# Kernel optimization log

Measured on AMD Instinct MI355X. Metric: run time of the kernel, lower is better.

## Reference

```python
import jax, jax.numpy as jnp
import numpy as np

TIME_STEPS = 50
LEFT_PAD = 250 // TIME_STEPS            # 5
MAX_DELAY = LEFT_PAD if LEFT_PAD % 2 == 1 else LEFT_PAD + 1  # 5 (odd)
SIG = float(MAX_DELAY // 2)             # 2.0, frozen
CIN = 34 * 34 * 2                       # 2312
HID = 300
NOUT = 10
BETA = 0.9
THRESH = 1.0
BATCH = 128


def setup_inputs() -> dict:
    key = jax.random.key(0)
    k = jax.random.split(key, 6)
    data = jax.random.normal(k[0], (BATCH, TIME_STEPS, CIN), jnp.float32)
    W1 = jax.random.normal(k[1], (HID, CIN), jnp.float32) / np.sqrt(CIN * MAX_DELAY).astype(np.float32)
    P1 = jax.random.uniform(k[2], (HID, CIN), jnp.float32, -SIG, SIG)
    b1 = jnp.zeros((HID,), jnp.float32)
    W2 = jax.random.normal(k[3], (NOUT, HID), jnp.float32) / np.sqrt(HID * MAX_DELAY).astype(np.float32)
    P2 = jax.random.uniform(k[4], (NOUT, HID), jnp.float32, -SIG, SIG)
    b2 = jnp.zeros((NOUT,), jnp.float32)
    return {"data": data, "W1": W1, "P1": P1, "b1": b1, "W2": W2, "P2": P2, "b2": b2}


def make_gauss_kernel(W, P):
    # DCLS 'gauss': weight W placed at learnable position P (centered at KS//2)
    # with Gaussian of width SIG, normalized over the KS taps. kernel_count=1.
    idx = jnp.arange(MAX_DELAY, dtype=W.dtype)              # [KS]
    c = P[..., None] + (MAX_DELAY // 2)                     # [O, I, 1]
    g = jnp.exp(-0.5 * ((idx - c) / SIG) ** 2)              # [O, I, KS]
    g = g / (g.sum(-1, keepdims=True) + 1e-7)
    return W[..., None] * g                                 # [O, I, KS]


def delay_conv(x, W, P, b):
    # x: [B, Cin, L], valid conv with synthesized kernel -> [B, Cout, L-KS+1]
    K = make_gauss_kernel(W, P)
    y = jax.lax.conv_general_dilated(x, K, window_strides=(1,), padding='VALID',
                                     dimension_numbers=('NCH', 'OIH', 'NCH'))
    return y + b[None, :, None]


def lif_scan(x):
    # snntorch Leaky (reset-by-subtraction, reset detached):
    #   mem_t = beta*mem_{t-1} + x_t - H(mem_{t-1}-thr)*thr ;  spk_t = H(mem_t-thr)
    # x: [B, C, T] -> (spk [T,B,C], mem [T,B,C])
    def step(mem, xt):
        reset = (mem > THRESH).astype(xt.dtype)
        mem_new = BETA * mem + xt - reset * THRESH
        spk = (mem_new > THRESH).astype(xt.dtype)
        return mem_new, (spk, mem_new)

    xs = jnp.moveaxis(x, 2, 0)                              # [T, B, C]
    mem0 = jnp.zeros(x.shape[:2], x.dtype)
    _, (spks, mems) = jax.lax.scan(step, mem0, xs)
    return spks, mems


def reference(data, W1, P1, b1, W2, P2, b2):
    # pad time (dim -2) on the left, permute to [B, Cin, T+pad]
    x = jnp.pad(data, ((0, 0), (LEFT_PAD, 0), (0, 0)))
    x = jnp.transpose(x, (0, 2, 1))                         # [B, CIN, T+pad]
    x = delay_conv(x, W1, P1, b1)                           # [B, HID, T1]
    spk1, _ = lif_scan(x)                                   # [T1, B, HID]
    h = jnp.moveaxis(spk1, 0, 2)                            # [B, HID, T1]
    h = jnp.pad(h, ((0, 0), (0, 0), (LEFT_PAD, 0)))
    y = delay_conv(h, W2, P2, b2)                           # [B, NOUT, T2]
    spk2, mem2 = lif_scan(y)                                # [T2, B, NOUT] each
    return spk2, mem2
```

## Files before the change

kernel.cpp:

```cpp
#include <hip/hip_runtime.h>

#define BSZ  128
#define TT   50
#define CIN  2312
#define HID  300
#define NOUT 10
#define KS   5
#define T1   51
#define T2   52

#define NC32 73
#define KFRAG_U 20480

typedef unsigned int u32;
typedef unsigned short u16;
typedef __attribute__((ext_vector_type(8))) short s16x8;
typedef __attribute__((ext_vector_type(4))) float f32x4;

#define EK1f 0.88249690258459546f
#define EK2f 0.60653065971263342f
#define EK3f 0.32465246735834974f
#define EK4f 0.13533528323661270f

static __device__ __forceinline__ u16 bfhi(float x) {
  u32 u = __float_as_uint(x);
  return (u16)((u + 0x7fffu + ((u >> 16) & 1u)) >> 16);
}
static __device__ __forceinline__ float bf2f(u16 h) {
  return __uint_as_float(((u32)h) << 16);
}

__global__ __launch_bounds__(256) void snn_prepm(
    const float* __restrict__ W1, const float* __restrict__ P1,
    u16* __restrict__ K1bf)
{
  const int c  = blockIdx.x;
  const int ow = blockIdx.y;
  const int tid = threadIdx.x;
  const int nt = tid >> 6, ll = tid & 63;
  const int g = ll >> 4, lr = ll & 15;
  const int o  = ow * 64 + nt * 16 + lr;
  const int ib = c * 32 + g * 8;

  s16x8 hv[5], lv[5];
#pragma unroll
  for (int k = 0; k < 5; ++k)
#pragma unroll
    for (int j = 0; j < 8; ++j) { hv[k][j] = 0; lv[k][j] = 0; }

  if (o < HID) {
    const float* wrow = W1 + (size_t)o * CIN;
    const float* prow = P1 + (size_t)o * CIN;
#pragma unroll
    for (int j = 0; j < 8; ++j) {
      const int i = ib + j;
      if (i < CIN) {
        const float w1 = wrow[i], p1 = prow[i];
        const float cc = p1 + 2.0f;
        const float E0 = __expf(-0.125f * cc * cc);
        const float U  = __expf(0.25f * cc);
        const float u2 = U * U;
        const float e0 = E0;
        const float e1 = E0 * U * EK1f;
        const float e2 = E0 * u2 * EK2f;
        const float e3 = E0 * (u2 * U) * EK3f;
        const float e4 = E0 * (u2 * u2) * EK4f;
        const float inv = 1.0f / (((((e0 + e1) + e2) + e3) + e4) + 1e-7f);
        const float vk[5] = { w1 * (e0 * inv), w1 * (e1 * inv),
                              w1 * (e2 * inv), w1 * (e3 * inv),
                              w1 * (e4 * inv) };
#pragma unroll
        for (int k = 0; k < 5; ++k) {
          const u16 h = bfhi(vk[k]);
          const u16 lo = bfhi(vk[k] - bf2f(h));
          hv[k][j] = (short)h; lv[k][j] = (short)lo;
        }
      }
    }
  }
  u16* base = K1bf + ((size_t)ow * NC32 + c) * KFRAG_U + nt * 1024 + ll * 8;
#pragma unroll
  for (int k = 0; k < 5; ++k) {
    *(s16x8*)(base + k * 4096)       = hv[k];
    *(s16x8*)(base + k * 4096 + 512) = lv[k];
  }
}

__global__ __launch_bounds__(256, 2) void snn_l1m(
    const float* __restrict__ data, const u16* __restrict__ K1bf,
    const float* __restrict__ b1v, u32* __restrict__ gbits)
{
  __shared__ double dsm[3264];
  u16* A16 = (u16*)dsm;

  const int tid = threadIdx.x;
  const int bid = blockIdx.x;
  const int rnk = (bid & 7) * 80 + (bid >> 3);
  const int ow = rnk >> 7;
  const int b  = rnk & 127;

  const int w  = tid >> 6, l = tid & 63;
  const int lr = l & 15, lg = l >> 4;
  const int wr = w >> 1, wc = w & 1;
  const int abase_u = (32 * wr + lr) * 40 + lg * 8;

  const float* dbase = data + (size_t)b * (TT * CIN);
  const u16* kb = K1bf + (size_t)ow * NC32 * KFRAG_U + l * 8;
  const int ntg0 = wc * 2, ntg1 = wc * 2 + 1;

  const int s1 = tid >> 2;
  const int j4 = tid & 3;
  const int tp = s1 - 5;
  const bool avld = (tp >= 0) && (tp < TT);
  const float* aptr = dbase + (size_t)(avld ? tp : 0) * CIN + j4 * 8;

#define LDB(c_, k_, ntg_, h_) \
  (*(const s16x8*)(kb + (size_t)(c_) * KFRAG_U + (k_) * 4096 + (ntg_) * 1024 + (h_) * 512))

  s16x8 bh[5][2], bl[5][2];
#pragma unroll
  for (int k = 0; k < 5; ++k) {
    bh[k][0] = LDB(0, k, ntg0, 0); bh[k][1] = LDB(0, k, ntg1, 0);
    bl[k][0] = LDB(0, k, ntg0, 1); bl[k][1] = LDB(0, k, ntg1, 1);
  }

  float4 ra0, ra1;
  {
    ra0 = avld ? *(const float4*)(aptr)     : make_float4(0.f, 0.f, 0.f, 0.f);
    ra1 = avld ? *(const float4*)(aptr + 4) : make_float4(0.f, 0.f, 0.f, 0.f);
  }

  if (tid < 80) {
    s16x8 z;
#pragma unroll
    for (int j = 0; j < 8; ++j) z[j] = 0;
    const int r = tid / 20, off = (tid % 20) * 8;
    *(s16x8*)(A16 + r * 2720 + 2560 + off) = z;
  }

  {
    const float f[8] = { ra0.x, ra0.y, ra0.z, ra0.w,
                         ra1.x, ra1.y, ra1.z, ra1.w };
    s16x8 hv, lv;
#pragma unroll
    for (int j = 0; j < 8; ++j) {
      const u16 h = bfhi(f[j]);
      hv[j] = (short)h;
      lv[j] = (short)bfhi(f[j] - bf2f(h));
    }
    *(s16x8*)(A16 + s1 * 40 + j4 * 8) = hv;
    *(s16x8*)(A16 + 2720 + s1 * 40 + j4 * 8) = lv;
  }
  {
    const bool iv = avld;
    const float* p = aptr + 32;
    ra0 = iv ? *(const float4*)(p)     : make_float4(0.f, 0.f, 0.f, 0.f);
    ra1 = iv ? *(const float4*)(p + 4) : make_float4(0.f, 0.f, 0.f, 0.f);
  }
  __syncthreads();

  f32x4 accf[2][2];
  double accd[2][2][4];
#pragma unroll
  for (int m = 0; m < 2; ++m)
#pragma unroll
    for (int n = 0; n < 2; ++n)
#pragma unroll
      for (int q = 0; q < 4; ++q) { accf[m][n][q] = 0.f; accd[m][n][q] = 0.0; }

  int p = 0;
  for (int c = 0; c < NC32; ++c) {
    u16* bufC = A16 + p * 2720 * 2;
    u16* bufN = A16 + (p ^ 1) * 2720 * 2;

    if (c + 1 < NC32) {
      const float f[8] = { ra0.x, ra0.y, ra0.z, ra0.w,
                           ra1.x, ra1.y, ra1.z, ra1.w };
      s16x8 hv, lv;
#pragma unroll
      for (int j = 0; j < 8; ++j) {
        const u16 h = bfhi(f[j]);
        hv[j] = (short)h;
        lv[j] = (short)bfhi(f[j] - bf2f(h));
      }
      *(s16x8*)(bufN + s1 * 40 + j4 * 8) = hv;
      *(s16x8*)(bufN + 2720 + s1 * 40 + j4 * 8) = lv;

      const int cn = (c + 2 < NC32) ? c + 2 : NC32 - 1;
      const bool iv = avld && ((cn < 72) || (j4 == 0));
      const float* pp = aptr + cn * 32;
      ra0 = iv ? *(const float4*)(pp)     : make_float4(0.f, 0.f, 0.f, 0.f);
      ra1 = iv ? *(const float4*)(pp + 4) : make_float4(0.f, 0.f, 0.f, 0.f);
    }

    const int cb = (c + 1 < NC32) ? c + 1 : c;
#pragma unroll
    for (int k = 0; k < 5; ++k) {
      const s16x8 ah0 = *(const s16x8*)(bufC + abase_u + k * 40);
      const s16x8 al0 = *(const s16x8*)(bufC + 2720 + abase_u + k * 40);
      const s16x8 ah1 = *(const s16x8*)(bufC + abase_u + (16 + k) * 40);
      const s16x8 al1 = *(const s16x8*)(bufC + 2720 + abase_u + (16 + k) * 40);

      accf[0][0] = __builtin_amdgcn_mfma_f32_16x16x32_bf16(ah0, bh[k][0], accf[0][0], 0, 0, 0);
      accf[0][0] = __builtin_amdgcn_mfma_f32_16x16x32_bf16(al0, bh[k][0], accf[0][0], 0, 0, 0);
      accf[0][0] = __builtin_amdgcn_mfma_f32_16x16x32_bf16(ah0, bl[k][0], accf[0][0], 0, 0, 0);

      accf[0][1] = __builtin_amdgcn_mfma_f32_16x16x32_bf16(ah0, bh[k][1], accf[0][1], 0, 0, 0);
      accf[0][1] = __builtin_amdgcn_mfma_f32_16x16x32_bf16(al0, bh[k][1], accf[0][1], 0, 0, 0);
      accf[0][1] = __builtin_amdgcn_mfma_f32_16x16x32_bf16(ah0, bl[k][1], accf[0][1], 0, 0, 0);

      accf[1][0] = __builtin_amdgcn_mfma_f32_16x16x32_bf16(ah1, bh[k][0], accf[1][0], 0, 0, 0);
      accf[1][0] = __builtin_amdgcn_mfma_f32_16x16x32_bf16(al1, bh[k][0], accf[1][0], 0, 0, 0);
      accf[1][0] = __builtin_amdgcn_mfma_f32_16x16x32_bf16(ah1, bl[k][0], accf[1][0], 0, 0, 0);

      accf[1][1] = __builtin_amdgcn_mfma_f32_16x16x32_bf16(ah1, bh[k][1], accf[1][1], 0, 0, 0);
      accf[1][1] = __builtin_amdgcn_mfma_f32_16x16x32_bf16(al1, bh[k][1], accf[1][1], 0, 0, 0);
      accf[1][1] = __builtin_amdgcn_mfma_f32_16x16x32_bf16(ah1, bl[k][1], accf[1][1], 0, 0, 0);

      bh[k][0] = LDB(cb, k, ntg0, 0); bh[k][1] = LDB(cb, k, ntg1, 0);
      bl[k][0] = LDB(cb, k, ntg0, 1); bl[k][1] = LDB(cb, k, ntg1, 1);
    }

#pragma unroll
    for (int m = 0; m < 2; ++m)
#pragma unroll
      for (int n = 0; n < 2; ++n)
#pragma unroll
        for (int q = 0; q < 4; ++q) {
          accd[m][n][q] += (double)accf[m][n][q];
          accf[m][n][q] = 0.f;
        }
    __syncthreads();
    p ^= 1;
  }
#undef LDB

  double* y1s = dsm;
#pragma unroll
  for (int m = 0; m < 2; ++m)
#pragma unroll
    for (int n = 0; n < 2; ++n)
#pragma unroll
      for (int q = 0; q < 4; ++q) {
        const int t = 32 * wr + 16 * m + lg * 4 + q;
        if (t < T1) y1s[t * 64 + 32 * wc + 16 * n + lr] = accd[m][n][q];
      }
  __syncthreads();

  if (tid < 64) {
    const int o = ow * 64 + tid;
    const bool valid = o < HID;
    const double bias = valid ? (double)b1v[o] : 0.0;
    u32* bits = gbits + (size_t)b * 510;
    double mem = 0.0;
    for (int t = 0; t < T1; ++t) {
      const double x = y1s[t * 64 + tid] + bias;
      const double reset = (mem > 1.0) ? 1.0 : 0.0;
      mem = __dsub_rn(__dadd_rn(__dmul_rn(0.9, mem), x), reset);
      const unsigned long long mk = __ballot(valid && (mem > 1.0));
      if (tid == 0)  bits[t * 10 + 2 * ow]     = (u32)mk;
      if (tid == 32) bits[t * 10 + 2 * ow + 1] = (u32)(mk >> 32);
    }
  }
}

__device__ __forceinline__ void layer1_tile_g(
    int b, int ow, int tid,
    const float* __restrict__ data, const float* __restrict__ W1,
    const float* __restrict__ P1, const float* __restrict__ b1v,
    double* __restrict__ dsm, u32* __restrict__ bits)
{
  float* Bsf = (float*)dsm;
  float* As  = (float*)dsm + 2880;

  const int ty = tid >> 5;
  const int tx = tid & 31;
  const int r0 = ty << 3;
  const int c0 = tx << 1;

  const float* abase = data + (size_t)b * (TT * CIN);

  const int slot = tid >> 2;
  const int pair = tid & 3;
  const int tp   = slot - 5;

  const int isub = tid & 7;
  const int oA = tid >> 3;
  const int oB = oA + 32;
  const int boA = ow * 64 + oA;
  const int boB = ow * 64 + oB;
  const bool vB = boB < HID;

  double acc[8][2];
#pragma unroll
  for (int r = 0; r < 8; ++r) { acc[r][0] = 0.0; acc[r][1] = 0.0; }

  float2 aA = make_float2(0.f, 0.f);
  float wA = 0.f, pA = 0.f, wB = 0.f, pB = 0.f;
  if (tid < 220 && tp >= 0)
    aA = *(const float2*)(abase + (size_t)tp * CIN + 2 * pair);
  wA = W1[(size_t)boA * CIN + isub];
  pA = P1[(size_t)boA * CIN + isub];
  if (vB) {
    wB = W1[(size_t)boB * CIN + isub];
    pB = P1[(size_t)boB * CIN + isub];
  }

  for (int i0 = 0; i0 < CIN; i0 += 8) {
    if (tid < 220) {
      As[(2 * pair) * 80 + slot]     = aA.x;
      As[(2 * pair + 1) * 80 + slot] = aA.y;
    }
    {
      const float c  = pA + 2.0f;
      const float E0 = __expf(-0.125f * c * c);
      const float U  = __expf(0.25f * c);
      const float u2 = U * U;
      const float e0 = E0;
      const float e1 = E0 * U * EK1f;
      const float e2 = E0 * u2 * EK2f;
      const float e3 = E0 * (u2 * U) * EK3f;
      const float e4 = E0 * (u2 * u2) * EK4f;
      const float inv = 1.0f / (((((e0 + e1) + e2) + e3) + e4) + 1e-7f);
      float* bp = Bsf + isub * 72 + oA;
      bp[0]    = wA * (e0 * inv);
      bp[576]  = wA * (e1 * inv);
      bp[1152] = wA * (e2 * inv);
      bp[1728] = wA * (e3 * inv);
      bp[2304] = wA * (e4 * inv);
    }
    {
      const float c  = pB + 2.0f;
      const float E0 = __expf(-0.125f * c * c);
      const float U  = __expf(0.25f * c);
      const float u2 = U * U;
      const float e0 = E0;
      const float e1 = E0 * U * EK1f;
      const float e2 = E0 * u2 * EK2f;
      const float e3 = E0 * (u2 * U) * EK3f;
      const float e4 = E0 * (u2 * u2) * EK4f;
      const float inv = 1.0f / (((((e0 + e1) + e2) + e3) + e4) + 1e-7f);
      float* bp = Bsf + isub * 72 + oB;
      bp[0]    = wB * (e0 * inv);
      bp[576]  = wB * (e1 * inv);
      bp[1152] = wB * (e2 * inv);
      bp[1728] = wB * (e3 * inv);
      bp[2304] = wB * (e4 * inv);
    }
    __syncthreads();

    const int i0n = i0 + 8;
    if (i0n < CIN) {
      if (tid < 220 && tp >= 0)
        aA = *(const float2*)(abase + (size_t)tp * CIN + i0n + 2 * pair);
      wA = W1[(size_t)boA * CIN + i0n + isub];
      pA = P1[(size_t)boA * CIN + i0n + isub];
      if (vB) {
        wB = W1[(size_t)boB * CIN + i0n + isub];
        pB = P1[(size_t)boB * CIN + i0n + isub];
      }
    }

    float accf[8][2];
#pragma unroll
    for (int r = 0; r < 8; ++r) { accf[r][0] = 0.f; accf[r][1] = 0.f; }
#pragma unroll
    for (int kk = 0; kk < 8; ++kk) {
      const float* ap = &As[kk * 80 + r0];
      const float4 a0 = *(const float4*)(ap);
      const float4 a1 = *(const float4*)(ap + 4);
      const float4 a2 = *(const float4*)(ap + 8);
      float av[12];
      av[0] = a0.x; av[1] = a0.y; av[2]  = a0.z; av[3]  = a0.w;
      av[4] = a1.x; av[5] = a1.y; av[6]  = a1.z; av[7]  = a1.w;
      av[8] = a2.x; av[9] = a2.y; av[10] = a2.z; av[11] = a2.w;
      float bv[KS][2];
#pragma unroll
      for (int k = 0; k < KS; ++k) {
        const float2 bb = *(const float2*)&Bsf[(k * 8 + kk) * 72 + c0];
        bv[k][0] = bb.x; bv[k][1] = bb.y;
      }
#pragma unroll
      for (int k = 0; k < KS; ++k)
#pragma unroll
        for (int r = 0; r < 8; ++r) {
          accf[r][0] = fmaf(av[r + k], bv[k][0], accf[r][0]);
          accf[r][1] = fmaf(av[r + k], bv[k][1], accf[r][1]);
        }
    }
#pragma unroll
    for (int r = 0; r < 8; ++r) {
      acc[r][0] += (double)accf[r][0];
      acc[r][1] += (double)accf[r][1];
    }
    __syncthreads();
  }

  double* y1s = dsm;
#pragma unroll
  for (int r = 0; r < 8; ++r) {
    const int t = r0 + r;
    if (t < T1) {
      y1s[t * 64 + c0]     = acc[r][0];
      y1s[t * 64 + c0 + 1] = acc[r][1];
    }
  }
  __syncthreads();

  if (tid < 64) {
    const int o = ow * 64 + tid;
    const bool valid = o < HID;
    const double bias = valid ? (double)b1v[o] : 0.0;
    double mem = 0.0;
    for (int t = 0; t < T1; ++t) {
      const double x = y1s[t * 64 + tid] + bias;
      const double reset = (mem > 1.0) ? 1.0 : 0.0;
      mem = __dsub_rn(__dadd_rn(__dmul_rn(0.9, mem), x), reset);
      const unsigned long long mk = __ballot(valid && (mem > 1.0));
      if (tid == 0)  bits[t * 10 + 2 * ow]     = (u32)mk;
      if (tid == 32) bits[t * 10 + 2 * ow + 1] = (u32)(mk >> 32);
    }
  }
  __syncthreads();
}

__device__ __forceinline__ void layer2_lif2(
    int b, int tid, float* smem,
    const float* __restrict__ W2, const float* __restrict__ P2,
    const float* __restrict__ b2, float* __restrict__ out)
{
  float* K2s = smem;
  const u32* lbits = (const u32*)(smem + 15000);
  float* y2s = smem + 15510;

  for (int idx = tid; idx < NOUT * HID; idx += 256) {
    const int o = idx / HID, i = idx % HID;
    const float w = W2[idx], p = P2[idx];
    const float c = p + 2.0f;
    float e[KS], s = 0.f;
#pragma unroll
    for (int k = 0; k < KS; ++k) {
      const float d = ((float)k - c) * 0.5f;
      e[k] = __expf(-0.5f * d * d);
      s += e[k];
    }
    const float denom = s + 1e-7f;
#pragma unroll
    for (int k = 0; k < KS; ++k)
      K2s[(o * KS + k) * HID + i] = w * (e[k] / denom);
  }
  __syncthreads();

  for (int task = tid; task < T2 * NOUT; task += 256) {
    const int t2 = task / NOUT, o = task % NOUT;
    float acc = b2[o];
#pragma unroll
    for (int k = 0; k < KS; ++k) {
      const int tp = t2 + k - KS;
      if (tp < 0 || tp >= T1) continue;
      const float* kr = K2s + (o * KS + k) * HID;
      const u32* br = lbits + tp * 10;
      for (int i = 0; i < HID; ++i)
        acc = fmaf((float)((br[i >> 5] >> (i & 31)) & 1u), kr[i], acc);
    }
    y2s[task] = acc;
  }
  __syncthreads();

  if (tid < NOUT) {
    float mem = 0.f;
    for (int t = 0; t < T2; ++t) {
      const float x = y2s[t * NOUT + tid];
      const float reset = (mem > 1.0f) ? 1.0f : 0.0f;
      mem = __fsub_rn(__fadd_rn(__fmul_rn(0.9f, mem), x), reset);
      out[(size_t)t * (BSZ * NOUT) + b * NOUT + tid] = (mem > 1.0f) ? 1.0f : 0.0f;
      out[(size_t)T2 * BSZ * NOUT + (size_t)t * (BSZ * NOUT) + b * NOUT + tid] = mem;
    }
  }
}

__global__ __launch_bounds__(256) void snn_l1(
    const float* __restrict__ data, const float* __restrict__ W1,
    const float* __restrict__ P1, const float* __restrict__ b1v,
    u32* __restrict__ gbits)
{
  __shared__ double dsm[3264];
  const int ow = blockIdx.x, b = blockIdx.y;
  layer1_tile_g(b, ow, threadIdx.x, data, W1, P1, b1v, dsm,
                gbits + (size_t)b * 510);
}

__global__ __launch_bounds__(256) void snn_l2k(
    const u32* __restrict__ gbits,
    const float* __restrict__ W2, const float* __restrict__ P2,
    const float* __restrict__ b2, float* __restrict__ out)
{
  __shared__ float smem[16030];
  const int b = blockIdx.x, tid = threadIdx.x;
  u32* lbits = (u32*)(smem + 15000);
  for (int i = tid; i < 510; i += 256) lbits[i] = gbits[(size_t)b * 510 + i];
  layer2_lif2(b, tid, smem, W2, P2, b2, out);
}

__global__ __launch_bounds__(256) void snn_mono(
    const float* __restrict__ data, const float* __restrict__ W1,
    const float* __restrict__ P1, const float* __restrict__ b1v,
    const float* __restrict__ W2, const float* __restrict__ P2,
    const float* __restrict__ b2, float* __restrict__ out)
{
  __shared__ double dsm[8015];
  const int b = blockIdx.x, tid = threadIdx.x;
  u32* lbits = (u32*)((float*)dsm + 15000);
  for (int ow = 0; ow < 5; ++ow)
    layer1_tile_g(b, ow, tid, data, W1, P1, b1v, dsm, lbits);
  layer2_lif2(b, tid, (float*)dsm, W2, P2, b2, out);
}

extern "C" void kernel_launch(void* const* d_in, const int* in_sizes, int n_in,
                              void* d_out, int out_size, void* d_ws, size_t ws_size,
                              hipStream_t stream) {
  const float* data = (const float*)d_in[0];
  const float* W1   = (const float*)d_in[1];
  const float* P1   = (const float*)d_in[2];
  const float* b1v  = (const float*)d_in[3];
  const float* W2   = (const float*)d_in[4];
  const float* P2   = (const float*)d_in[5];
  const float* b2   = (const float*)d_in[6];
  float* out = (float*)d_out;

  const size_t BITS_BYTES = (size_t)BSZ * T1 * 10 * sizeof(u32);
  const size_t K1_OFF = 262144;
  const size_t K1BF_BYTES = (size_t)5 * NC32 * KFRAG_U * 2;
  const size_t NEED_M = K1_OFF + K1BF_BYTES;

  if (ws_size >= NEED_M) {
    u32* gbits = (u32*)d_ws;
    u16* K1bf  = (u16*)((char*)d_ws + K1_OFF);
    snn_prepm<<<dim3(NC32, 5), 256, 0, stream>>>(W1, P1, K1bf);
    snn_l1m<<<640, 256, 0, stream>>>(data, K1bf, b1v, gbits);
    snn_l2k<<<BSZ, 256, 0, stream>>>(gbits, W2, P2, b2, out);
  } else if (ws_size >= BITS_BYTES) {
    u32* gbits = (u32*)d_ws;
    snn_l1<<<dim3(5, BSZ), 256, 0, stream>>>(data, W1, P1, b1v, gbits);
    snn_l2k<<<BSZ, 256, 0, stream>>>(gbits, W2, P2, b2, out);
  } else {
    snn_mono<<<BSZ, 256, 0, stream>>>(data, W1, P1, b1v, W2, P2, b2, out);
  }
}
```

Measured before the change: 401.4 us.

## Split layer-1 channel reduction in two and move LIF1 into layer-2 kernel

Adds a split-K variant of the layer-1 MFMA kernel that divides the 73 channel chunks between two blocks, launching 1280 blocks with a higher occupancy hint. Each block writes float partial sums to a workspace buffer. A new layer-2 kernel adds the two partials plus bias, runs the layer-1 LIF scan in double precision, and then does layer 2. The aim is more parallelism and better CU coverage for the large GEMM. The cost is extra global traffic for the partials, and rounding the per-half double accumulators to float could flip spikes near threshold. The old kernel is also tidied into the same load/stage macro structure.

New measurement: 984.7 us. +145.3%, slower.

```diff
diff --git a/kernel.cpp b/kernel.cpp
--- a/kernel.cpp
+++ b/kernel.cpp
@@ -86,6 +86,244 @@
   }
 }
 
+__global__ __launch_bounds__(256, 4) void snn_l1s(
+    const float* __restrict__ data, const u16* __restrict__ K1bf,
+    float* __restrict__ pbuf)
+{
+  __shared__ __align__(16) double dsm[2720];
+  u16* A16 = (u16*)dsm;
+
+  const int tid = threadIdx.x;
+  const int bid = blockIdx.x;
+  const int g  = bid & 7;
+  const int r  = bid >> 3;
+  const int s  = r & 1;
+  const int u  = r >> 1;
+  const int x  = g * 80 + u;
+  const int ow = x >> 7;
+  const int b  = x & 127;
+
+  const int c_lo = s ? 37 : 0;
+  const int c_hi = s ? 73 : 37;
+
+  const int w  = tid >> 6, l = tid & 63;
+  const int lr = l & 15, lg = l >> 4;
+  const int wr = w >> 1, wc = w & 1;
+  const int abase_u = (32 * wr + lr) * 40 + lg * 8;
+
+  const float* dbase = data + (size_t)b * (TT * CIN);
+  const u16* kbn = K1bf + (size_t)ow * NC32 * KFRAG_U + l * 8;
+  const int ntg0 = wc * 2, ntg1 = wc * 2 + 1;
+
+  const int s1 = tid >> 2;
+  const int j4 = tid & 3;
+  const int tp = s1 - 5;
+  const bool avld = (tp >= 0) && (tp < TT);
+  const float* aptr = dbase + (size_t)(avld ? tp : 0) * CIN + j4 * 8;
+
+  if (tid < 80) {
+    s16x8 z;
+#pragma unroll
+    for (int j = 0; j < 8; ++j) z[j] = 0;
+    const int rr = tid / 20, off = (tid % 20) * 8;
+    *(s16x8*)(A16 + rr * 2720 + 2560 + off) = z;
+  }
+
+#define LOADA(CC)                                                             \
+  {                                                                           \
+    const bool iv_ = avld && (((CC) < 72) || (j4 == 0));                      \
+    const float* pp_ = aptr + (size_t)(CC) * 32;                              \
+    ra0 = iv_ ? *(const float4*)(pp_)     : make_float4(0.f, 0.f, 0.f, 0.f);  \
+    ra1 = iv_ ? *(const float4*)(pp_ + 4) : make_float4(0.f, 0.f, 0.f, 0.f);  \
+  }
+
+#define STAGE_A(CC)                                                           \
+  {                                                                           \
+    const float f_[8] = { ra0.x, ra0.y, ra0.z, ra0.w,                         \
+                          ra1.x, ra1.y, ra1.z, ra1.w };                       \
+    s16x8 hv_, lv_;                                                           \
+    _Pragma("unroll")                                                         \
+    for (int j = 0; j < 8; ++j) {                                             \
+      const u16 h_ = bfhi(f_[j]);                                             \
+      hv_[j] = (short)h_;                                                     \
+      lv_[j] = (short)bfhi(f_[j] - bf2f(h_));                                 \
+    }                                                                         \
+    u16* bn_ = A16 + ((CC) & 1) * 5440;                                       \
+    const int woff_ = s1 * 40 + j4 * 8;                                       \
+    *(s16x8*)(bn_ + woff_) = hv_;                                             \
+    *(s16x8*)(bn_ + 2720 + woff_) = lv_;                                      \
+  }
+
+  s16x8 bh[5][2], bl[5][2];
+#pragma unroll
+  for (int k = 0; k < 5; ++k) {
+    const u16* cb_ = kbn + (size_t)c_lo * KFRAG_U + k * 4096;
+    bh[k][0] = *(const s16x8*)(cb_ + ntg0 * 1024);
+    bh[k][1] = *(const s16x8*)(cb_ + ntg1 * 1024);
+    bl[k][0] = *(const s16x8*)(cb_ + ntg0 * 1024 + 512);
+    bl[k][1] = *(const s16x8*)(cb_ + ntg1 * 1024 + 512);
+  }
+
+  f32x4 accf[2][2];
+  double accd[2][2][4];
+#pragma unroll
+  for (int m = 0; m < 2; ++m)
+#pragma unroll
+    for (int n = 0; n < 2; ++n)
+#pragma unroll
+      for (int q = 0; q < 4; ++q) { accf[m][n][q] = 0.f; accd[m][n][q] = 0.0; }
+
+  float4 ra0, ra1;
+  LOADA(c_lo);
+  STAGE_A(c_lo);
+  LOADA(c_lo + 1);
+  __syncthreads();
+
+  for (int c = c_lo; c < c_hi; ++c) {
+    if (c + 1 < c_hi) {
+      STAGE_A(c + 1);
+      if (c + 2 < c_hi) LOADA(c + 2);
+    }
+
+    {
+      const u16* bc_ = A16 + (c & 1) * 5440;
+      const int rc = c + 1;
+#pragma unroll
+      for (int k = 0; k < 5; ++k) {
+        const s16x8 ah0 = *(const s16x8*)(bc_ + abase_u + k * 40);
+        const s16x8 al0 = *(const s16x8*)(bc_ + 2720 + abase_u + k * 40);
+        const s16x8 ah1 = *(const s16x8*)(bc_ + abase_u + (16 + k) * 40);
+        const s16x8 al1 = *(const s16x8*)(bc_ + 2720 + abase_u + (16 + k) * 40);
+
+        accf[0][0] = __builtin_amdgcn_mfma_f32_16x16x32_bf16(ah0, bh[k][0], accf[0][0], 0, 0, 0);
+        accf[0][0] = __builtin_amdgcn_mfma_f32_16x16x32_bf16(al0, bh[k][0], accf[0][0], 0, 0, 0);
+        accf[0][0] = __builtin_amdgcn_mfma_f32_16x16x32_bf16(ah0, bl[k][0], accf[0][0], 0, 0, 0);
+
+        accf[0][1] = __builtin_amdgcn_mfma_f32_16x16x32_bf16(ah0, bh[k][1], accf[0][1], 0, 0, 0);
+        accf[0][1] = __builtin_amdgcn_mfma_f32_16x16x32_bf16(al0, bh[k][1], accf[0][1], 0, 0, 0);
+        accf[0][1] = __builtin_amdgcn_mfma_f32_16x16x32_bf16(ah0, bl[k][1], accf[0][1], 0, 0, 0);
+
+        accf[1][0] = __builtin_amdgcn_mfma_f32_16x16x32_bf16(ah1, bh[k][0], accf[1][0], 0, 0, 0);
+        accf[1][0] = __builtin_amdgcn_mfma_f32_16x16x32_bf16(al1, bh[k][0], accf[1][0], 0, 0, 0);
+        accf[1][0] = __builtin_amdgcn_mfma_f32_16x16x32_bf16(ah1, bl[k][0], accf[1][0], 0, 0, 0);
+
+        accf[1][1] = __builtin_amdgcn_mfma_f32_16x16x32_bf16(ah1, bh[k][1], accf[1][1], 0, 0, 0);
+        accf[1][1] = __builtin_amdgcn_mfma_f32_16x16x32_bf16(al1, bh[k][1], accf[1][1], 0, 0, 0);
+        accf[1][1] = __builtin_amdgcn_mfma_f32_16x16x32_bf16(ah1, bl[k][1], accf[1][1], 0, 0, 0);
+
+        if (rc < c_hi) {
+          const u16* cb_ = kbn + (size_t)rc * KFRAG_U + k * 4096;
+          bh[k][0] = *(const s16x8*)(cb_ + ntg0 * 1024);
+          bh[k][1] = *(const s16x8*)(cb_ + ntg1 * 1024);
+          bl[k][0] = *(const s16x8*)(cb_ + ntg0 * 1024 + 512);
+          bl[k][1] = *(const s16x8*)(cb_ + ntg1 * 1024 + 512);
+        }
+      }
+    }
+
+#pragma unroll
+    for (int m = 0; m < 2; ++m)
+#pragma unroll
+      for (int n = 0; n < 2; ++n)
+#pragma unroll
+        for (int q = 0; q < 4; ++q) {
+          accd[m][n][q] += (double)accf[m][n][q];
+          accf[m][n][q] = 0.f;
+        }
+    __syncthreads();
+  }
+#undef LOADA
+#undef STAGE_A
+
+  float* pb = pbuf + (((size_t)s * 5 + ow) * 128 + b) * 3264;
+#pragma unroll
+  for (int m = 0; m < 2; ++m)
+#pragma unroll
+    for (int n = 0; n < 2; ++n)
+#pragma unroll
+      for (int q = 0; q < 4; ++q) {
+        const int t = 32 * wr + 16 * m + lg * 4 + q;
+        if (t < T1) pb[t * 64 + 32 * wc + 16 * n + lr] = (float)accd[m][n][q];
+      }
+}
+
+__global__ __launch_bounds__(256) void snn_l2m(
+    const float* __restrict__ pbuf, const float* __restrict__ b1v,
+    const float* __restrict__ W2, const float* __restrict__ P2,
+    const float* __restrict__ b2, float* __restrict__ out)
+{
+  __shared__ float smem[16030];
+  const int b = blockIdx.x, tid = threadIdx.x;
+  float* K2s = smem;
+  u32* lbits = (u32*)(smem + 15000);
+  float* y2s = smem + 15510;
+
+  for (int idx = tid; idx < NOUT * HID; idx += 256) {
+    const int o = idx / HID, i = idx % HID;
+    const float w = W2[idx], p = P2[idx];
+    const float c = p + 2.0f;
+    float e[KS], ssum = 0.f;
+#pragma unroll
+    for (int k = 0; k < KS; ++k) {
+      const float d = ((float)k - c) * 0.5f;
+      e[k] = __expf(-0.5f * d * d);
+      ssum += e[k];
+    }
+    const float denom = ssum + 1e-7f;
+#pragma unroll
+    for (int k = 0; k < KS; ++k)
+      K2s[(o * KS + k) * HID + i] = w * (e[k] / denom);
+  }
+
+  {
+    const int w = tid >> 6, l = tid & 63;
+    for (int ow = w; ow < 5; ow += 4) {
+      const int o = ow * 64 + l;
+      const bool valid = o < HID;
+      const double bias = valid ? (double)b1v[o] : 0.0;
+      const float* p0 = pbuf + (((size_t)0 * 5 + ow) * 128 + b) * 3264 + l;
+      const float* p1 = pbuf + (((size_t)1 * 5 + ow) * 128 + b) * 3264 + l;
+      double mem = 0.0;
+      for (int t = 0; t < T1; ++t) {
+        const double x = (double)p0[t * 64] + (double)p1[t * 64] + bias;
+        const double reset = (mem > 1.0) ? 1.0 : 0.0;
+        mem = __dsub_rn(__dadd_rn(__dmul_rn(0.9, mem), x), reset);
+        const unsigned long long mk = __ballot(valid && (mem > 1.0));
+        if (l == 0)  lbits[t * 10 + 2 * ow]     = (u32)mk;
+        if (l == 32) lbits[t * 10 + 2 * ow + 1] = (u32)(mk >> 32);
+      }
+    }
+  }
+  __syncthreads();
+
+  for (int task = tid; task < T2 * NOUT; task += 256) {
+    const int t2 = task / NOUT, o = task % NOUT;
+    float acc = b2[o];
+#pragma unroll
+    for (int k = 0; k < KS; ++k) {
+      const int tp = t2 + k - KS;
+      if (tp < 0 || tp >= T1) continue;
+      const float* kr = K2s + (o * KS + k) * HID;
+      const u32* br = lbits + tp * 10;
+      for (int i = 0; i < HID; ++i)
+        acc = fmaf((float)((br[i >> 5] >> (i & 31)) & 1u), kr[i], acc);
+    }
+    y2s[task] = acc;
+  }
+  __syncthreads();
+
+  if (tid < NOUT) {
+    float mem = 0.f;
+    for (int t = 0; t < T2; ++t) {
+      const float x = y2s[t * NOUT + tid];
+      const float reset = (mem > 1.0f) ? 1.0f : 0.0f;
+      mem = __fsub_rn(__fadd_rn(__fmul_rn(0.9f, mem), x), reset);
+      out[(size_t)t * (BSZ * NOUT) + b * NOUT + tid] = (mem > 1.0f) ? 1.0f : 0.0f;
+      out[(size_t)T2 * BSZ * NOUT + (size_t)t * (BSZ * NOUT) + b * NOUT + tid] = mem;
+    }
+  }
+}
+
 __global__ __launch_bounds__(256, 2) void snn_l1m(
     const float* __restrict__ data, const u16* __restrict__ K1bf,
     const float* __restrict__ b1v, u32* __restrict__ gbits)
@@ -105,7 +343,7 @@
   const int abase_u = (32 * wr + lr) * 40 + lg * 8;
 
   const float* dbase = data + (size_t)b * (TT * CIN);
-  const u16* kb = K1bf + (size_t)ow * NC32 * KFRAG_U + l * 8;
+  const u16* kbn = K1bf + (size_t)ow * NC32 * KFRAG_U + l * 8;
   const int ntg0 = wc * 2, ntg1 = wc * 2 + 1;
 
   const int s1 = tid >> 2;
@@ -114,50 +352,48 @@
   const bool avld = (tp >= 0) && (tp < TT);
   const float* aptr = dbase + (size_t)(avld ? tp : 0) * CIN + j4 * 8;
 
-#define LDB(c_, k_, ntg_, h_) \
-  (*(const s16x8*)(kb + (size_t)(c_) * KFRAG_U + (k_) * 4096 + (ntg_) * 1024 + (h_) * 512))
-
-  s16x8 bh[5][2], bl[5][2];
-#pragma unroll
-  for (int k = 0; k < 5; ++k) {
-    bh[k][0] = LDB(0, k, ntg0, 0); bh[k][1] = LDB(0, k, ntg1, 0);
-    bl[k][0] = LDB(0, k, ntg0, 1); bl[k][1] = LDB(0, k, ntg1, 1);
-  }
-
-  float4 ra0, ra1;
-  {
-    ra0 = avld ? *(const float4*)(aptr)     : make_float4(0.f, 0.f, 0.f, 0.f);
-    ra1 = avld ? *(const float4*)(aptr + 4) : make_float4(0.f, 0.f, 0.f, 0.f);
-  }
-
   if (tid < 80) {
     s16x8 z;
 #pragma unroll
     for (int j = 0; j < 8; ++j) z[j] = 0;
-    const int r = tid / 20, off = (tid % 20) * 8;
-    *(s16x8*)(A16 + r * 2720 + 2560 + off) = z;
-  }
-
-  {
-    const float f[8] = { ra0.x, ra0.y, ra0.z, ra0.w,
-                         ra1.x, ra1.y, ra1.z, ra1.w };
-    s16x8 hv, lv;
-#pragma unroll
-    for (int j = 0; j < 8; ++j) {
-      const u16 h = bfhi(f[j]);
-      hv[j] = (short)h;
-      lv[j] = (short)bfhi(f[j] - bf2f(h));
-    }
-    *(s16x8*)(A16 + s1 * 40 + j4 * 8) = hv;
-    *(s16x8*)(A16 + 2720 + s1 * 40 + j4 * 8) = lv;
-  }
-  {
-    const bool iv = avld;
-    const float* p = aptr + 32;
-    ra0 = iv ? *(const float4*)(p)     : make_float4(0.f, 0.f, 0.f, 0.f);
-    ra1 = iv ? *(const float4*)(p + 4) : make_float4(0.f, 0.f, 0.f, 0.f);
-  }
-  __syncthreads();
+    const int rr = tid / 20, off = (tid % 20) * 8;
+    *(s16x8*)(A16 + rr * 2720 + 2560 + off) = z;
+  }
+
+#define LOADA(CC)                                                             \
+  {                                                                           \
+    const bool iv_ = avld && (((CC) < 72) || (j4 == 0));                      \
+    const float* pp_ = aptr + (size_t)(CC) * 32;                              \
+    ra0 = iv_ ? *(const float4*)(pp_)     : make_float4(0.f, 0.f, 0.f, 0.f);  \
+    ra1 = iv_ ? *(const float4*)(pp_ + 4) : make_float4(0.f, 0.f, 0.f, 0.f);  \
+  }
+
+#define STAGE_A(CC)                                                           \
+  {                                                                           \
+    const float f_[8] = { ra0.x, ra0.y, ra0.z, ra0.w,                         \
+                          ra1.x, ra1.y, ra1.z, ra1.w };                       \
+    s16x8 hv_, lv_;                                                           \
+    _Pragma("unroll")                                                         \
+    for (int j = 0; j < 8; ++j) {                                             \
+      const u16 h_ = bfhi(f_[j]);                                             \
+      hv_[j] = (short)h_;                                                     \
+      lv_[j] = (short)bfhi(f_[j] - bf2f(h_));                                 \
+    }                                                                         \
+    u16* bn_ = A16 + ((CC) & 1) * 5440;                                       \
+    const int woff_ = s1 * 40 + j4 * 8;                                       \
+    *(s16x8*)(bn_ + woff_) = hv_;                                             \
+    *(s16x8*)(bn_ + 2720 + woff_) = lv_;                                      \
+  }
+
+  s16x8 bh[5][2], bl[5][2];
+#pragma unroll
+  for (int k = 0; k < 5; ++k) {
+    const u16* cb_ = kbn + k * 4096;
+    bh[k][0] = *(const s16x8*)(cb_ + ntg0 * 1024);
+    bh[k][1] = *(const s16x8*)(cb_ + ntg1 * 1024);
+    bl[k][0] = *(const s16x8*)(cb_ + ntg0 * 1024 + 512);
+    bl[k][1] = *(const s16x8*)(cb_ + ntg1 * 1024 + 512);
+  }
 
   f32x4 accf[2][2];
   double accd[2][2][4];
@@ -168,59 +404,49 @@
 #pragma unroll
       for (int q = 0; q < 4; ++q) { accf[m][n][q] = 0.f; accd[m][n][q] = 0.0; }
 
-  int p = 0;
+  float4 ra0, ra1;
+  LOADA(0);
+  STAGE_A(0);
+  LOADA(1);
+  __syncthreads();
+
   for (int c = 0; c < NC32; ++c) {
-    u16* bufC = A16 + p * 2720 * 2;
-    u16* bufN = A16 + (p ^ 1) * 2720 * 2;
-
     if (c + 1 < NC32) {
-      const float f[8] = { ra0.x, ra0.y, ra0.z, ra0.w,
-                           ra1.x, ra1.y, ra1.z, ra1.w };
-      s16x8 hv, lv;
-#pragma unroll
-      for (int j = 0; j < 8; ++j) {
-        const u16 h = bfhi(f[j]);
-        hv[j] = (short)h;
-        lv[j] = (short)bfhi(f[j] - bf2f(h));
+      STAGE_A(c + 1);
+      if (c + 2 < NC32) LOADA(c + 2);
+    }
+    {
+      const u16* bc_ = A16 + (c & 1) * 5440;
+      const int rc = c + 1;
+#pragma unroll
+      for (int k = 0; k < 5; ++k) {
+        const s16x8 ah0 = *(const s16x8*)(bc_ + abase_u + k * 40);
+        const s16x8 al0 = *(const s16x8*)(bc_ + 2720 + abase_u + k * 40);
+        const s16x8 ah1 = *(const s16x8*)(bc_ + abase_u + (16 + k) * 40);
+        const s16x8 al1 = *(const s16x8*)(bc_ + 2720 + abase_u + (16 + k) * 40);
+
+        accf[0][0] = __builtin_amdgcn_mfma_f32_16x16x32_bf16(ah0, bh[k][0], accf[0][0], 0, 0, 0);
+        accf[0][0] = __builtin_amdgcn_mfma_f32_16x16x32_bf16(al0, bh[k][0], accf[0][0], 0, 0, 0);
+        accf[0][0] = __builtin_amdgcn_mfma_f32_16x16x32_bf16(ah0, bl[k][0], accf[0][0], 0, 0, 0);
+        accf[0][1] = __builtin_amdgcn_mfma_f32_16x16x32_bf16(ah0, bh[k][1], accf[0][1], 0, 0, 0);
+        accf[0][1] = __builtin_amdgcn_mfma_f32_16x16x32_bf16(al0, bh[k][1], accf[0][1], 0, 0, 0);
+        accf[0][1] = __builtin_amdgcn_mfma_f32_16x16x32_bf16(ah0, bl[k][1], accf[0][1], 0, 0, 0);
+        accf[1][0] = __builtin_amdgcn_mfma_f32_16x16x32_bf16(ah1, bh[k][0], accf[1][0], 0, 0, 0);
+        accf[1][0] = __builtin_amdgcn_mfma_f32_16x16x32_bf16(al1, bh[k][0], accf[1][0], 0, 0, 0);
+        accf[1][0] = __builtin_amdgcn_mfma_f32_16x16x32_bf16(ah1, bl[k][0], accf[1][0], 0, 0, 0);
+        accf[1][1] = __builtin_amdgcn_mfma_f32_16x16x32_bf16(ah1, bh[k][1], accf[1][1], 0, 0, 0);
+        accf[1][1] = __builtin_amdgcn_mfma_f32_16x16x32_bf16(al1, bh[k][1], accf[1][1], 0, 0, 0);
+        accf[1][1] = __builtin_amdgcn_mfma_f32_16x16x32_bf16(ah1, bl[k][1], accf[1][1], 0, 0, 0);
+
+        if (rc < NC32) {
+          const u16* cb_ = kbn + (size_t)rc * KFRAG_U + k * 4096;
+          bh[k][0] = *(const s16x8*)(cb_ + ntg0 * 1024);
+          bh[k][1] = *(const s16x8*)(cb_ + ntg1 * 1024);
+          bl[k][0] = *(const s16x8*)(cb_ + ntg0 * 1024 + 512);
+          bl[k][1] = *(const s16x8*)(cb_ + ntg1 * 1024 + 512);
+        }
       }
-      *(s16x8*)(bufN + s1 * 40 + j4 * 8) = hv;
-      *(s16x8*)(bufN + 2720 + s1 * 40 + j4 * 8) = lv;
-
-      const int cn = (c + 2 < NC32) ? c + 2 : NC32 - 1;
-      const bool iv = avld && ((cn < 72) || (j4 == 0));
-      const float* pp = aptr + cn * 32;
-      ra0 = iv ? *(const float4*)(pp)     : make_float4(0.f, 0.f, 0.f, 0.f);
-      ra1 = iv ? *(const float4*)(pp + 4) : make_float4(0.f, 0.f, 0.f, 0.f);
-    }
-
-    const int cb = (c + 1 < NC32) ? c + 1 : c;
-#pragma unroll
-    for (int k = 0; k < 5; ++k) {
-      const s16x8 ah0 = *(const s16x8*)(bufC + abase_u + k * 40);
-      const s16x8 al0 = *(const s16x8*)(bufC + 2720 + abase_u + k * 40);
-      const s16x8 ah1 = *(const s16x8*)(bufC + abase_u + (16 + k) * 40);
-      const s16x8 al1 = *(const s16x8*)(bufC + 2720 + abase_u + (16 + k) * 40);
-
-      accf[0][0] = __builtin_amdgcn_mfma_f32_16x16x32_bf16(ah0, bh[k][0], accf[0][0], 0, 0, 0);
-      accf[0][0] = __builtin_amdgcn_mfma_f32_16x16x32_bf16(al0, bh[k][0], accf[0][0], 0, 0, 0);
-      accf[0][0] = __builtin_amdgcn_mfma_f32_16x16x32_bf16(ah0, bl[k][0], accf[0][0], 0, 0, 0);
-
-      accf[0][1] = __builtin_amdgcn_mfma_f32_16x16x32_bf16(ah0, bh[k][1], accf[0][1], 0, 0, 0);
-      accf[0][1] = __builtin_amdgcn_mfma_f32_16x16x32_bf16(al0, bh[k][1], accf[0][1], 0, 0, 0);
-      accf[0][1] = __builtin_amdgcn_mfma_f32_16x16x32_bf16(ah0, bl[k][1], accf[0][1], 0, 0, 0);
-
-      accf[1][0] = __builtin_amdgcn_mfma_f32_16x16x32_bf16(ah1, bh[k][0], accf[1][0], 0, 0, 0);
-      accf[1][0] = __builtin_amdgcn_mfma_f32_16x16x32_bf16(al1, bh[k][0], accf[1][0], 0, 0, 0);
-      accf[1][0] = __builtin_amdgcn_mfma_f32_16x16x32_bf16(ah1, bl[k][0], accf[1][0], 0, 0, 0);
-
-      accf[1][1] = __builtin_amdgcn_mfma_f32_16x16x32_bf16(ah1, bh[k][1], accf[1][1], 0, 0, 0);
-      accf[1][1] = __builtin_amdgcn_mfma_f32_16x16x32_bf16(al1, bh[k][1], accf[1][1], 0, 0, 0);
-      accf[1][1] = __builtin_amdgcn_mfma_f32_16x16x32_bf16(ah1, bl[k][1], accf[1][1], 0, 0, 0);
-
-      bh[k][0] = LDB(cb, k, ntg0, 0); bh[k][1] = LDB(cb, k, ntg1, 0);
-      bl[k][0] = LDB(cb, k, ntg0, 1); bl[k][1] = LDB(cb, k, ntg1, 1);
-    }
-
+    }
 #pragma unroll
     for (int m = 0; m < 2; ++m)
 #pragma unroll
@@ -231,9 +457,9 @@
           accf[m][n][q] = 0.f;
         }
     __syncthreads();
-    p ^= 1;
-  }
-#undef LDB
+  }
+#undef LOADA
+#undef STAGE_A
 
   double* y1s = dsm;
 #pragma unroll
@@ -528,14 +754,22 @@
   const float* b2   = (const float*)d_in[6];
   float* out = (float*)d_out;
 
-  const size_t BITS_BYTES = (size_t)BSZ * T1 * 10 * sizeof(u32);
-  const size_t K1_OFF = 262144;
-  const size_t K1BF_BYTES = (size_t)5 * NC32 * KFRAG_U * 2;
-  const size_t NEED_M = K1_OFF + K1BF_BYTES;
-
-  if (ws_size >= NEED_M) {
+  const size_t BITS_BYTES  = (size_t)BSZ * T1 * 10 * sizeof(u32);
+  const size_t K1BF_BYTES  = (size_t)5 * NC32 * KFRAG_U * 2;
+  const size_t PBUF_BYTES  = (size_t)2 * 5 * 128 * 3264 * 4;
+  const size_t NEED_S = PBUF_BYTES + K1BF_BYTES;
+  const size_t K1_OFF_M = 262144;
+  const size_t NEED_M = K1_OFF_M + K1BF_BYTES;
+
+  if (ws_size >= NEED_S) {
+    float* pbuf = (float*)d_ws;
+    u16* K1bf   = (u16*)((char*)d_ws + PBUF_BYTES);
+    snn_prepm<<<dim3(NC32, 5), 256, 0, stream>>>(W1, P1, K1bf);
+    snn_l1s<<<1280, 256, 0, stream>>>(data, K1bf, pbuf);
+    snn_l2m<<<BSZ, 256, 0, stream>>>(pbuf, b1v, W2, P2, b2, out);
+  } else if (ws_size >= NEED_M) {
     u32* gbits = (u32*)d_ws;
-    u16* K1bf  = (u16*)((char*)d_ws + K1_OFF);
+    u16* K1bf  = (u16*)((char*)d_ws + K1_OFF_M);
     snn_prepm<<<dim3(NC32, 5), 256, 0, stream>>>(W1, P1, K1bf);
     snn_l1m<<<640, 256, 0, stream>>>(data, K1bf, b1v, gbits);
     snn_l2k<<<BSZ, 256, 0, stream>>>(gbits, W2, P2, b2, out);
```
